# Optimization experiments

Hardware: AMD Instinct MI355X
Metric: run time of the kernel (lower is better)

Reference implementation:

```python
import jax, jax.numpy as jnp
from jax import lax
import numpy as np

VOCAB, EMB, HID, ENC, ATT, P = 10000, 512, 1024, 2048, 512, 196
B, T = 64, 160
PAD_IDX = 3

def setup_inputs() -> dict:
    key = jax.random.key(0)
    ks = jax.random.split(key, 20)
    s = 0.02
    emb = jax.random.normal(ks[0], (VOCAB, EMB), jnp.float32) * s
    emb = emb.at[PAD_IDX].set(0.0)
    return {
        'image_embedding': jax.random.normal(ks[1], (B, P, ENC), jnp.float32),
        'padded_sentence': jax.random.randint(ks[2], (B, T), 0, VOCAB),
        'enc_h': jax.random.normal(ks[3], (2, B, HID // 2), jnp.float32),
        'enc_c': jax.random.normal(ks[4], (2, B, HID // 2), jnp.float32),
        'sentence_lens': jax.random.randint(ks[5], (B,), 1, T + 1),
        'emb': emb,
        'Wea': jax.random.normal(ks[6], (ATT, ENC), jnp.float32) * s,
        'bea': jnp.zeros((ATT,), jnp.float32),
        'Wda': jax.random.normal(ks[7], (ATT, HID), jnp.float32) * s,
        'bda': jnp.zeros((ATT,), jnp.float32),
        'wfa': jax.random.normal(ks[8], (ATT,), jnp.float32) * s,
        'bfa': jnp.zeros((), jnp.float32),
        'Wfb': jax.random.normal(ks[9], (ENC, HID), jnp.float32) * s,
        'bfb': jnp.zeros((ENC,), jnp.float32),
        'Wih': jax.random.normal(ks[10], (4 * HID, EMB + ENC), jnp.float32) * s,
        'bih': jnp.zeros((4 * HID,), jnp.float32),
        'Whh': jax.random.normal(ks[11], (4 * HID, HID), jnp.float32) * s,
        'bhh': jnp.zeros((4 * HID,), jnp.float32),
    }


def reference(image_embedding, padded_sentence, enc_h, enc_c, sentence_lens,
              emb, Wea, bea, Wda, bda, wfa, bfa, Wfb, bfb, Wih, bih, Whh, bhh):
    Tn = padded_sentence.shape[1]
    # sort by descending length (replicates sentence_lens.sort(descending=True))
    idx = jnp.argsort(-sentence_lens)
    img = image_embedding[idx]                   # [B,P,E]
    sent = padded_sentence[idx]                  # [B,T]
    lens = sentence_lens[idx]                    # [B]
    h0 = jnp.concatenate([enc_h[-2], enc_h[-1]], axis=1)[idx]  # [B,HID]
    c0 = jnp.concatenate([enc_c[-2], enc_c[-1]], axis=1)[idx]
    emb_eff = emb.at[PAD_IDX].set(0.0)           # padding_idx=3
    x_emb = emb_eff[sent]                        # [B,T,EMB]
    # encoder projection is h-independent: hoist out of the scan
    att1 = jnp.einsum('bpe,ae->bpa', img, Wea) + bea  # [B,P,ATT]

    def step(carry, xt):
        h, c = carry
        x_t, t = xt
        active = (t < lens)[:, None]             # ragged mask
        att2 = h @ Wda.T + bda                   # [B,ATT]
        e = jax.nn.relu(att1 + att2[:, None, :]) @ wfa + bfa  # [B,P]
        alpha = jax.nn.softmax(e, axis=1)
        context = jnp.einsum('bp,bpe->be', alpha, img)        # [B,ENC]
        gate = jax.nn.sigmoid(h @ Wfb.T + bfb)
        inp = jnp.concatenate([x_t, gate * context], axis=1)  # [B,EMB+ENC]
        gates = inp @ Wih.T + bih + h @ Whh.T + bhh           # [B,4*HID]
        i, f, g, o = jnp.split(gates, 4, axis=1)
        c_new = jax.nn.sigmoid(f) * c + jax.nn.sigmoid(i) * jnp.tanh(g)
        h_new = jax.nn.sigmoid(o) * jnp.tanh(c_new)
        h = jnp.where(active, h_new, h)
        c = jnp.where(active, c_new, c)
        out_t = jnp.where(active, h_new, 0.0)
        alpha_t = jnp.where(active, alpha, 0.0)
        return (h, c), (out_t, alpha_t)

    (_, _), (outs, alphas) = lax.scan(
        step, (h0, c0), (jnp.swapaxes(x_emb, 0, 1), jnp.arange(Tn)))
    outputs = jnp.swapaxes(outs, 0, 1)           # [B,T,HID]
    alphas = jnp.swapaxes(alphas, 0, 1)          # [B,T,P]
    # replicate the original's final reindex (outputs[ordered_idx], not inverse)
    return outputs[idx], alphas[idx]
```

## Files before the change

kernel.cpp:

```cpp
#include <hip/hip_runtime.h>
#include <hip/hip_bf16.h>
#include <math.h>

#define B 64
#define T 160
#define P 196
#define ENC 2048
#define ATT 512
#define EMB 512
#define HID 1024
#define KTOT 3584
#define N2 2560
#define KT4 112
#define NTHR 1024
#define NBLK 256
#define NGRP 16
#define GRPSZ (NBLK/NGRP)

#define ARR_W 0
#define GD_W  16384
#define REL_W 17408

typedef __attribute__((ext_vector_type(8))) short bf16x8;
typedef __attribute__((ext_vector_type(4))) float f32x4;
typedef __attribute__((ext_vector_type(2))) float f32x2;

__device__ __forceinline__ float sigm(float x){ return 1.0f/(1.0f+__expf(-x)); }
__device__ __forceinline__ float bfu(short s){ return __uint_as_float(((unsigned)(unsigned short)s) << 16); }
__device__ __forceinline__ short f2bf(float x){ __hip_bfloat16 h = __float2bfloat16(x); return *(short*)&h; }

#if __has_builtin(__builtin_amdgcn_cvt_pk_f32_fp8)
#define FP8_DEC2(w, sel) __builtin_amdgcn_cvt_pk_f32_fp8((int)(w), (sel))
#else
__device__ __forceinline__ float fp8dec1(unsigned b){
    unsigned s = b >> 7, e = (b >> 3) & 15, m = b & 7;
    float v = e ? __uint_as_float(((e + 120u) << 23) | (m << 20)) : (float)(int)m * 0.001953125f;
    return s ? -v : v;
}
__device__ __forceinline__ f32x2 FP8_DEC2(unsigned w, int sel){
    unsigned h = sel ? (w >> 16) : (w & 0xFFFFu);
    f32x2 r; r.x = fp8dec1(h & 0xFF); r.y = fp8dec1(h >> 8);
    return r;
}
#endif

__device__ __forceinline__ unsigned char fp8enc(float x){
    unsigned bits = __float_as_uint(x);
    unsigned s = (bits >> 31) << 7;
    unsigned abits = bits & 0x7FFFFFFFu;
    float a = __uint_as_float(abits);
    if (a >= 448.f) return (unsigned char)(s | 0x7E);
    if (a < 0.0009765625f) return (unsigned char)s;
    int E = (int)(abits >> 23) - 127;
    if (E < -6){
        int q = (int)rintf(a * 512.0f);
        if (q >= 8) return (unsigned char)(s | 0x08);
        return (unsigned char)(s | q);
    }
    unsigned m23 = abits & 0x7FFFFFu;
    unsigned r = (m23 + 0x7FFFFu + ((m23 >> 20) & 1u)) >> 20;
    if (r >= 8){ r = 0; E++; }
    if (E > 8 || (E == 8 && r > 6)) return (unsigned char)(s | 0x7E);
    return (unsigned char)(s | ((unsigned)(E + 7) << 3) | r);
}

__device__ __forceinline__ float ldgf(const float* p){ return *(const volatile float*)p; }
__device__ __forceinline__ void stgf(float* p, float v){ *(volatile float*)p = v; }
__device__ __forceinline__ void stgu(unsigned* p, unsigned v){ *(volatile unsigned*)p = v; }
__device__ __forceinline__ unsigned pkbf(float a, float b){
    unsigned ua = (unsigned)__bfloat16_as_ushort(__float2bfloat16(a));
    unsigned ub = (unsigned)__bfloat16_as_ushort(__float2bfloat16(b));
    return ua | (ub << 16);
}

__device__ __forceinline__ void gbar_arrive(unsigned* bar, unsigned k){
    asm volatile("s_waitcnt vmcnt(0)" ::: "memory");
    __syncthreads();
    if (threadIdx.x == 0)
        *(volatile unsigned*)(bar + ARR_W + (unsigned)blockIdx.x*64) = k + 1u;
}
__device__ __forceinline__ void gbar_wait(unsigned* bar, unsigned k){
    int b = blockIdx.x, tid = threadIdx.x;
    if (b < NGRP){
        if (tid < 64){
            volatile unsigned* s = (volatile unsigned*)(bar + ARR_W + (unsigned)((tid & 15)*NGRP + b)*64);
            while (!__all(*s >= k + 1u)) __builtin_amdgcn_s_sleep(1);
            if (tid == 0) *(volatile unsigned*)(bar + GD_W + b*64) = k + 1u;
            volatile unsigned* g = (volatile unsigned*)(bar + GD_W + (tid & 15)*64);
            while (!__all(*g >= k + 1u)) __builtin_amdgcn_s_sleep(1);
            if (tid == 0) *(volatile unsigned*)(bar + REL_W + b*64) = k + 1u;
        }
    } else {
        if (tid == 0){
            volatile unsigned* r = (volatile unsigned*)(bar + REL_W + (b & (NGRP-1))*64);
            while (*r < k + 1u) __builtin_amdgcn_s_sleep(1);
        }
    }
    __syncthreads();
    asm volatile("" ::: "memory");
}
__device__ __forceinline__ void gbar(unsigned* bar, unsigned k){
    gbar_arrive(bar, k);
    gbar_wait(bar, k);
}

__global__ void k_sort(const int* lens, int* idx, int* rank, unsigned* barCnt, int* nAct){
    __shared__ int L[B];
    int i = threadIdx.x;
    L[i] = lens[i];
    for (int s = i; s < 288; s += B){
        int wofs = (s < 256) ? (ARR_W + s*64)
                 : (s < 272) ? (GD_W + (s-256)*64)
                             : (REL_W + (s-272)*64);
        barCnt[wofs] = 0u;
    }
    __syncthreads();
    int li = L[i];
    int r = 0;
    for (int j = 0; j < B; ++j){
        int lj = L[j];
        if (lj > li || (lj == li && j < i)) r++;
    }
    rank[i] = r;
    idx[r] = i;
    for (int tt = i; tt < T; tt += B){
        int c = 0;
        for (int j = 0; j < B; ++j) c += (L[j] > tt) ? 1 : 0;
        nAct[tt] = c;
    }
}

__global__ void k_init_hc(const float* enc_h, const float* enc_c, const int* idx,
                          float* h, float* c, __hip_bfloat16* hbR0){
    int j = blockIdx.x;
    int o = idx[j];
    for (int k = threadIdx.x; k < HID; k += blockDim.x){
        float hv = (k < 512) ? enc_h[o*512 + k] : enc_h[B*512 + o*512 + (k-512)];
        float cv = (k < 512) ? enc_c[o*512 + k] : enc_c[B*512 + o*512 + (k-512)];
        h[j*HID + k] = hv;
        c[j*HID + k] = cv;
        hbR0[j*HID + k] = __float2bfloat16(hv);
    }
}

__global__ void k_cvt_wcat(const float* Wih, const float* Whh, __hip_bfloat16* Wfrag){
    size_t i = (size_t)blockIdx.x*256 + threadIdx.x;
    int e = (int)(i & 7);
    size_t t2 = i >> 3;
    int lane = (int)(t2 & 63);
    size_t t3 = t2 >> 6;
    int kt = (int)(t3 % KT4);
    int strip = (int)(t3 / KT4);
    int n = strip*16 + (lane & 15);
    int r = (n & 3)*HID + (n >> 2);
    int k = kt*32 + (lane >> 4)*8 + e;
    float v = (k < EMB+ENC) ? Wih[(size_t)r*(EMB+ENC) + k]
                            : Whh[(size_t)r*HID + (k - EMB - ENC)];
    Wfrag[i] = __float2bfloat16(v);
}

__global__ void k_bsum(const float* bih, const float* bhh, float* bsum){
    int n = blockIdx.x*256 + threadIdx.x;
    int r = (n & 3)*HID + (n >> 2);
    bsum[n] = bih[r] + bhh[r];
}

__global__ void k_cvt_w2(const float* Wda, const float* bda, const float* Wfb, const float* bfb,
                         __hip_bfloat16* W2, float* bias2){
    int n = blockIdx.x;
    const float* src = (n < ATT) ? (Wda + (size_t)n*HID) : (Wfb + (size_t)(n-ATT)*HID);
    __hip_bfloat16* dst = W2 + (size_t)n*HID;
    for (int k = threadIdx.x; k < HID; k += 256) dst[k] = __float2bfloat16(src[k]);
    if (threadIdx.x == 0) bias2[n] = (n < ATT) ? bda[n] : bfb[n-ATT];
}

__global__ void k_cvt_emb(const float* emb, __hip_bfloat16* emb_bf){
    size_t i = (size_t)blockIdx.x*256 + threadIdx.x;
    emb_bf[i] = __float2bfloat16(emb[i]);
}

__global__ void k_cvt_wea(const float* Wea, __hip_bfloat16* Wea_bf){
    int n = blockIdx.x;
    for (int k = threadIdx.x; k < ENC; k += 256)
        Wea_bf[(size_t)n*ENC + k] = __float2bfloat16(Wea[(size_t)n*ENC + k]);
}

__global__ void k_cvt_img8(const float* img, const int* idx, unsigned char* img8){
    int j = blockIdx.y;
    int o = idx[j];
    size_t off = (size_t)blockIdx.x*256 + threadIdx.x;
    img8[(size_t)j*P*ENC + off] = fp8enc(img[(size_t)o*P*ENC + off]);
}

__global__ __launch_bounds__(256) void k_att1m(const float* img, const int* idx,
                                               const __hip_bfloat16* Wea_bf,
                                               const float* bea, __hip_bfloat16* att1w){
    int m0 = blockIdx.x * 64, n0 = blockIdx.y * 64;
    int tid = threadIdx.x, w = tid >> 6, l = tid & 63, lm = l & 15, lk = l >> 4;
    int g = m0 + 16*w + lm;
    int j = g / P, pp2 = g - j*P;
    int o = idx[j];
    const float* af = img + ((size_t)o*P + pp2)*ENC + 8*lk;
    const short* bp = (const short*)Wea_bf + (size_t)(n0 + lm)*ENC + 8*lk;
    f32x4 acc[4];
    #pragma unroll
    for (int nt=0; nt<4; ++nt) acc[nt] = (f32x4){0.f,0.f,0.f,0.f};
    #pragma unroll 4
    for (int kt = 0; kt < ENC/32; ++kt){
        float4 f0 = *(const float4*)(af + kt*32);
        float4 f1 = *(const float4*)(af + kt*32 + 4);
        bf16x8 a;
        a[0]=f2bf(f0.x); a[1]=f2bf(f0.y); a[2]=f2bf(f0.z); a[3]=f2bf(f0.w);
        a[4]=f2bf(f1.x); a[5]=f2bf(f1.y); a[6]=f2bf(f1.z); a[7]=f2bf(f1.w);
        #pragma unroll
        for (int nt=0; nt<4; ++nt){
            bf16x8 bb = *(const bf16x8*)(bp + (size_t)nt*16*ENC + kt*32);
            acc[nt] = __builtin_amdgcn_mfma_f32_16x16x32_bf16(a, bb, acc[nt], 0,0,0);
        }
    }
    #pragma unroll
    for (int nt=0; nt<4; ++nt){
        int n = n0 + nt*16 + lm;
        float bv = bea[n];
        #pragma unroll
        for (int r=0; r<4; ++r){
            int m = m0 + 16*w + 4*lk + r;
            att1w[(size_t)m*ATT + n] = __float2bfloat16(acc[nt][r] + bv);
        }
    }
}

struct SP {
    const __hip_bfloat16 *att1w, *emb_bf, *Wfrag, *W2;
    const unsigned char *img8;
    const float *bsum, *bias2, *wfa, *bfa;
    const int *sent, *idx, *rank, *lens, *nAct;
    float *D2;
    __hip_bfloat16 *gcR, *hbR;
    float *hF0, *hF1, *cW;
    float *outH, *outA;
    unsigned *barCnt;
};

__global__ __launch_bounds__(1024, 4) void k_scan(SP p){
    __shared__ short WcatL[KT4*64*8];
    __shared__ union {
        struct { float Dp[4][64][17]; float hS[64][4]; int tokL[64], lensL[64], wLs[64]; } gem;
        struct { float att2L[512]; float wfaL[512]; float red[1024]; float aL[208]; float ctxP[8][512]; } p23;
    } sh;

    int b = blockIdx.x, tid = threadIdx.x;
    int w = tid >> 6, l = tid & 63, lm = l & 15, lk = l >> 4;
    unsigned bk = 0;

    {
        const bf16x8* src = (const bf16x8*)((const short*)p.Wfrag + (size_t)b*KT4*64*8);
        bf16x8* dst = (bf16x8*)WcatL;
        #pragma unroll
        for (int i = 0; i < KT4*64/NTHR; ++i) dst[tid + i*NTHR] = src[tid + i*NTHR];
    }
    __syncthreads();

    float bfa0 = p.bfa[0];

    for (int t = 0; t < T; ++t){
        const __hip_bfloat16* hbIn = p.hbR + (size_t)t*B*HID;
        __hip_bfloat16*       hbOut = p.hbR + (size_t)(t+1)*B*HID;
        const __hip_bfloat16* gcT  = p.gcR + (size_t)t*B*ENC;
        const float* hFIn = (t & 1) ? p.hF1 : p.hF0;
        float*       hFOut = (t & 1) ? p.hF0 : p.hF1;
        int nAct = p.nAct[t];

        if (b < N2/16){
            int n0 = b*16;
            int rt = w & 3, kq = w >> 2;
            if (16*rt < nAct){
                const short* ap = (const short*)hbIn + (size_t)(16*rt + lm)*HID + kq*256 + 8*lk;
                const short* bp = (const short*)p.W2 + (size_t)(n0 + lm)*HID + kq*256 + 8*lk;
                f32x4 acc = {0.f,0.f,0.f,0.f};
                #pragma unroll
                for (int kt = 0; kt < 8; ++kt){
                    bf16x8 a = *(const bf16x8*)(ap + kt*32);
                    bf16x8 bb = *(const bf16x8*)(bp + kt*32);
                    acc = __builtin_amdgcn_mfma_f32_16x16x32_bf16(a, bb, acc, 0,0,0);
                }
                #pragma unroll
                for (int r=0; r<4; ++r) sh.gem.Dp[kq][16*rt + 4*lk + r][lm] = acc[r];
            }
            __syncthreads();
            int m = tid >> 4, nl = tid & 15;
            if (m < nAct){
                stgf(&p.D2[m*N2 + n0 + nl],
                     sh.gem.Dp[0][m][nl] + sh.gem.Dp[1][m][nl]
                   + sh.gem.Dp[2][m][nl] + sh.gem.Dp[3][m][nl] + p.bias2[n0 + nl]);
            }
        }
        gbar(p.barCnt, bk); bk++;

        int jj = b & 63, qq = b >> 6;
        int oo = p.idx[jj], wjj = p.rank[jj], ljj = p.lens[oo];
        {
            if (t < ljj){
                if (tid < 512){
                    sh.p23.att2L[tid] = ldgf(&p.D2[jj*N2 + tid]);
                    sh.p23.wfaL[tid]  = p.wfa[tid];
                }
                __syncthreads();

                int pp = tid & 255, ah = tid >> 8;
                float acc = 0.f;
                if (pp < P){
                    const short* ar = (const short*)p.att1w + (size_t)(jj*P + pp)*ATT + ah*128;
                    #pragma unroll 8
                    for (int k8 = 0; k8 < 16; ++k8){
                        bf16x8 v = *(const bf16x8*)(ar + k8*8);
                        #pragma unroll
                        for (int z=0; z<8; ++z){
                            int a = ah*128 + k8*8 + z;
                            acc += fmaxf(bfu(v[z]) + sh.p23.att2L[a], 0.f) * sh.p23.wfaL[a];
                        }
                    }
                }
                sh.p23.red[tid] = acc;
                __syncthreads();
                float e = -1e30f;
                if (tid < P) e = sh.p23.red[tid] + sh.p23.red[tid+256] + sh.p23.red[tid+512] + sh.p23.red[tid+768] + bfa0;
                __syncthreads();
                sh.p23.red[tid] = (tid < P) ? e : -1e30f;
                __syncthreads();
                for (int s = 512; s > 0; s >>= 1){
                    if (tid < s) sh.p23.red[tid] = fmaxf(sh.p23.red[tid], sh.p23.red[tid+s]);
                    __syncthreads();
                }
                float m = sh.p23.red[0];
                __syncthreads();
                float ex = (tid < P) ? __expf(e - m) : 0.f;
                sh.p23.red[tid] = ex;
                __syncthreads();
                for (int s = 512; s > 0; s >>= 1){
                    if (tid < s) sh.p23.red[tid] += sh.p23.red[tid+s];
                    __syncthreads();
                }
                float ssum = sh.p23.red[0];
                if (tid < P) sh.p23.aL[tid] = ex / ssum;
                if (tid >= P && tid < 208) sh.p23.aL[tid] = 0.f;
                __syncthreads();

                const unsigned char* ib = p.img8 + (size_t)jj*P*ENC + qq*512 + l*8;
                float a8[8];
                #pragma unroll
                for (int z=0; z<8; ++z) a8[z] = 0.f;
                #pragma unroll 4
                for (int i = 0; i < 13; ++i){
                    int pp2 = w + 16*i;
                    int pr = (pp2 < P) ? pp2 : 0;
                    uint2 v = *(const uint2*)(ib + (size_t)pr*ENC);
                    float al = sh.p23.aL[pp2];
                    f32x2 f01 = FP8_DEC2(v.x, 0);
                    f32x2 f23 = FP8_DEC2(v.x, 1);
                    f32x2 f45 = FP8_DEC2(v.y, 0);
                    f32x2 f67 = FP8_DEC2(v.y, 1);
                    a8[0] += al * f01.x; a8[1] += al * f01.y;
                    a8[2] += al * f23.x; a8[3] += al * f23.y;
                    a8[4] += al * f45.x; a8[5] += al * f45.y;
                    a8[6] += al * f67.x; a8[7] += al * f67.y;
                }
                if (w < 8){
                    #pragma unroll
                    for (int z=0; z<8; ++z) sh.p23.ctxP[w][l*8+z] = a8[z];
                }
                __syncthreads();
                if (w >= 8){
                    #pragma unroll
                    for (int z=0; z<8; ++z) sh.p23.ctxP[w-8][l*8+z] += a8[z];
                }
                __syncthreads();
                if (tid < 256){
                    int d0 = 2*tid;
                    float c0 = 0.f, c1 = 0.f;
                    #pragma unroll
                    for (int r=0; r<8; ++r){ c0 += sh.p23.ctxP[r][d0]; c1 += sh.p23.ctxP[r][d0+1]; }
                    int eg0 = qq*512 + d0;
                    float g0 = sigm(ldgf(&p.D2[jj*N2 + ATT + eg0]));
                    float g1 = sigm(ldgf(&p.D2[jj*N2 + ATT + eg0 + 1]));
                    stgu((unsigned*)((short*)gcT + jj*ENC + eg0), pkbf(g0*c0, g1*c1));
                }
            }
        }
        gbar_arrive(p.barCnt, bk);

        if (qq == 0 && tid < P){
            float av = (t < ljj) ? sh.p23.aL[tid] : 0.f;
            p.outA[((size_t)(wjj*T + t))*P + tid] = av;
        }
        __syncthreads();

        if (tid < 64){
            int o = p.idx[tid];
            sh.gem.tokL[tid] = p.sent[o*T + t];
            sh.gem.lensL[tid] = p.lens[o];
            sh.gem.wLs[tid] = p.rank[tid];
        }
        __syncthreads();
        {
            int rt = w & 3, kq = w >> 2;
            bool act = (16*rt < nAct);
            int mrow = 16*rt + lm;
            f32x4 acc = {0.f,0.f,0.f,0.f};
            const short* aEmb = 0; const short* aGc = 0; const short* aH = 0;
            const bf16x8* BL = (const bf16x8*)WcatL;
            if (act){
                int tok = sh.gem.tokL[mrow];
                aEmb = (const short*)p.emb_bf + (size_t)tok*EMB + 8*lk;
                aGc  = (const short*)gcT + (size_t)mrow*ENC + 8*lk;
                aH   = (const short*)hbIn + (size_t)mrow*HID + 8*lk;
                if (kq == 0){
                    #pragma unroll 8
                    for (int kt = 0; kt < 16; ++kt){
                        bf16x8 a = *(const bf16x8*)(aEmb + kt*32);
                        acc = __builtin_amdgcn_mfma_f32_16x16x32_bf16(a, BL[kt*64 + l], acc, 0,0,0);
                    }
                } else if (kq == 2){
                    #pragma unroll
                    for (int kt = 80; kt < 84; ++kt){
                        bf16x8 a = *(const bf16x8*)(aH + (kt-80)*32);
                        acc = __builtin_amdgcn_mfma_f32_16x16x32_bf16(a, BL[kt*64 + l], acc, 0,0,0);
                    }
                } else if (kq == 3){
                    #pragma unroll 7
                    for (int kt = 84; kt < 112; ++kt){
                        bf16x8 a = *(const bf16x8*)(aH + (kt-80)*32);
                        acc = __builtin_amdgcn_mfma_f32_16x16x32_bf16(a, BL[kt*64 + l], acc, 0,0,0);
                    }
                }
            }
            gbar_wait(p.barCnt, bk); bk++;

            if (act){
                if (kq == 0){
                    #pragma unroll 6
                    for (int kt = 16; kt < 28; ++kt){
                        bf16x8 a = *(const bf16x8*)(aGc + (kt-16)*32);
                        acc = __builtin_amdgcn_mfma_f32_16x16x32_bf16(a, BL[kt*64 + l], acc, 0,0,0);
                    }
                } else if (kq == 1){
                    #pragma unroll 7
                    for (int kt = 28; kt < 56; ++kt){
                        bf16x8 a = *(const bf16x8*)(aGc + (kt-16)*32);
                        acc = __builtin_amdgcn_mfma_f32_16x16x32_bf16(a, BL[kt*64 + l], acc, 0,0,0);
                    }
                } else if (kq == 2){
                    #pragma unroll 6
                    for (int kt = 56; kt < 80; ++kt){
                        bf16x8 a = *(const bf16x8*)(aGc + (kt-16)*32);
                        acc = __builtin_amdgcn_mfma_f32_16x16x32_bf16(a, BL[kt*64 + l], acc, 0,0,0);
                    }
                }
                #pragma unroll
                for (int r=0; r<4; ++r) sh.gem.Dp[kq][16*rt + 4*lk + r][lm] = acc[r];
            }
        }
        __syncthreads();

        int j2 = tid & 63, du = tid >> 6;
        int u = 4*b + du;
        float cNew = 0.f, hNew = 0.f, hKeep = 0.f, cOld = 0.f;
        bool active = false;
        if (tid < 256){
            float g4[4];
            #pragma unroll
            for (int g=0; g<4; ++g){
                int nl = 4*du + g;
                g4[g] = sh.gem.Dp[0][j2][nl] + sh.gem.Dp[1][j2][nl]
                      + sh.gem.Dp[2][j2][nl] + sh.gem.Dp[3][j2][nl] + p.bsum[16*b + nl];
            }
            float ig = sigm(g4[0]), fg = sigm(g4[1]), gg = tanhf(g4[2]), og = sigm(g4[3]);
            cOld = p.cW[j2*HID + u];
            cNew = fg*cOld + ig*gg;
            hNew = og*tanhf(cNew);
            active = (t < sh.gem.lensL[j2]);
            float hOld = hFIn[j2*HID + u];
            hKeep = active ? hNew : hOld;
            sh.gem.hS[j2][du] = hKeep;
        }
        __syncthreads();
        if (tid < 128){
            int jb = tid & 63, dp = tid >> 6;
            int u0 = 4*b + 2*dp;
            stgu((unsigned*)((short*)hbOut + jb*HID + u0),
                 pkbf(sh.gem.hS[jb][2*dp], sh.gem.hS[jb][2*dp+1]));
        }
        gbar_arrive(p.barCnt, bk);
        if (tid < 256){
            p.cW[j2*HID + u] = active ? cNew : cOld;
            hFOut[j2*HID + u] = hKeep;
            p.outH[((size_t)sh.gem.wLs[j2]*T + t)*HID + u] = active ? hNew : 0.f;
        }
        gbar_wait(p.barCnt, bk); bk++;
    }
}

extern "C" void kernel_launch(void* const* d_in, const int* in_sizes, int n_in,
                              void* d_out, int out_size, void* d_ws, size_t ws_size,
                              hipStream_t stream) {
    const float* img   = (const float*)d_in[0];
    const int*   sent  = (const int*)  d_in[1];
    const float* enc_h = (const float*)d_in[2];
    const float* enc_c = (const float*)d_in[3];
    const int*   lens  = (const int*)  d_in[4];
    const float* emb   = (const float*)d_in[5];
    const float* Wea   = (const float*)d_in[6];
    const float* bea   = (const float*)d_in[7];
    const float* Wda   = (const float*)d_in[8];
    const float* bda   = (const float*)d_in[9];
    const float* wfa   = (const float*)d_in[10];
    const float* bfa   = (const float*)d_in[11];
    const float* Wfb   = (const float*)d_in[12];
    const float* bfb   = (const float*)d_in[13];
    const float* Wih   = (const float*)d_in[14];
    const float* bih   = (const float*)d_in[15];
    const float* Whh   = (const float*)d_in[16];
    const float* bhh   = (const float*)d_in[17];

    float* outH = (float*)d_out;
    float* outA = outH + (size_t)B*T*HID;

    char* wsb = (char*)d_ws;
    size_t off = 0;
    int* idxW  = (int*)(wsb + off); off += 256;
    int* rankW = (int*)(wsb + off); off += 256;
    int* nActW = (int*)(wsb + off); off += 1024;
    unsigned* barCnt = (unsigned*)(wsb + off); off += 131072;
    __hip_bfloat16* att1w = (__hip_bfloat16*)(wsb + off); off += (size_t)B*P*ATT*2;
    unsigned char* img8 = (unsigned char*)(wsb + off); off += (size_t)B*P*ENC;
    __hip_bfloat16* emb_bf= (__hip_bfloat16*)(wsb + off); off += (size_t)10000*EMB*2;
    __hip_bfloat16* Wfrag = (__hip_bfloat16*)(wsb + off); off += (size_t)4*HID*KTOT*2;
    __hip_bfloat16* W2    = (__hip_bfloat16*)(wsb + off); off += (size_t)N2*HID*2;
    __hip_bfloat16* Wea_bf= (__hip_bfloat16*)(wsb + off); off += (size_t)ATT*ENC*2;
    float* bsum  = (float*)(wsb + off); off += 4*HID*4;
    float* bias2 = (float*)(wsb + off); off += N2*4;
    float* hA    = (float*)(wsb + off); off += B*HID*4;
    float* hB    = (float*)(wsb + off); off += B*HID*4;
    float* cWs   = (float*)(wsb + off); off += B*HID*4;
    float* D2    = (float*)(wsb + off); off += (size_t)B*N2*4;
    __hip_bfloat16* gcR = (__hip_bfloat16*)(wsb + off); off += (size_t)T*B*ENC*2;
    __hip_bfloat16* hbR = (__hip_bfloat16*)(wsb + off); off += (size_t)(T+1)*B*HID*2;

    k_sort<<<1, 64, 0, stream>>>(lens, idxW, rankW, barCnt, nActW);
    k_init_hc<<<B, 256, 0, stream>>>(enc_h, enc_c, idxW, hA, cWs, hbR);
    k_cvt_wcat<<<57344, 256, 0, stream>>>(Wih, Whh, Wfrag);
    k_bsum<<<16, 256, 0, stream>>>(bih, bhh, bsum);
    k_cvt_w2<<<N2, 256, 0, stream>>>(Wda, bda, Wfb, bfb, W2, bias2);
    k_cvt_emb<<<20000, 256, 0, stream>>>(emb, emb_bf);
    k_cvt_wea<<<ATT, 256, 0, stream>>>(Wea, Wea_bf);
    k_cvt_img8<<<dim3(P*ENC/256, B), 256, 0, stream>>>(img, idxW, img8);
    k_att1m<<<dim3((B*P)/64, ATT/64), 256, 0, stream>>>(img, idxW, Wea_bf, bea, att1w);

    SP sp;
    sp.att1w = att1w; sp.img8 = img8; sp.emb_bf = emb_bf; sp.Wfrag = Wfrag; sp.W2 = W2;
    sp.bsum = bsum; sp.bias2 = bias2; sp.wfa = wfa; sp.bfa = bfa;
    sp.sent = sent; sp.idx = idxW; sp.rank = rankW; sp.lens = lens; sp.nAct = nActW;
    sp.D2 = D2; sp.gcR = gcR; sp.hbR = hbR;
    sp.hF0 = hA; sp.hF1 = hB; sp.cW = cWs;
    sp.outH = outH; sp.outA = outA;
    sp.barCnt = barCnt;

    void* args[] = { &sp };
    hipLaunchCooperativeKernel(reinterpret_cast<void*>(k_scan), dim3(NBLK), dim3(NTHR),
                               args, 0, stream);
}
```

Before: 6.884 ms.

## Replace grid-wide barriers with per-producer dataflow flags and wave-shuffle softmax

The three hierarchical grid barriers per timestep are replaced by per-block monotonic progress flags. Each consumer wave polls only the blocks that produce the data it needs: the h slices for the recurrent GEMM, the D2 columns for attention, and all gated-context producers before the LSTM gate GEMM. Blocks can therefore start a phase as soon as their own inputs are ready instead of waiting for every block at every phase. The softmax max and sum tree reductions over 1024 shared-memory slots are also replaced with 64-lane shuffles plus a 4-entry combine, removing many __syncthreads. Correctness now relies on the flag ordering to cover the write-after-read hazards on D2 and hbR.

```diff
diff --git a/kernel.cpp b/kernel.cpp
--- a/kernel.cpp
+++ b/kernel.cpp
@@ -14,12 +14,6 @@
 #define KT4 112
 #define NTHR 1024
 #define NBLK 256
-#define NGRP 16
-#define GRPSZ (NBLK/NGRP)
-
-#define ARR_W 0
-#define GD_W  16384
-#define REL_W 17408
 
 typedef __attribute__((ext_vector_type(8))) short bf16x8;
 typedef __attribute__((ext_vector_type(4))) float f32x4;
@@ -73,47 +67,37 @@
     return ua | (ub << 16);
 }
 
-__device__ __forceinline__ void gbar_arrive(unsigned* bar, unsigned k){
+__device__ __forceinline__ void arrive(unsigned* bar, unsigned pi){
     asm volatile("s_waitcnt vmcnt(0)" ::: "memory");
     __syncthreads();
     if (threadIdx.x == 0)
-        *(volatile unsigned*)(bar + ARR_W + (unsigned)blockIdx.x*64) = k + 1u;
-}
-__device__ __forceinline__ void gbar_wait(unsigned* bar, unsigned k){
-    int b = blockIdx.x, tid = threadIdx.x;
-    if (b < NGRP){
-        if (tid < 64){
-            volatile unsigned* s = (volatile unsigned*)(bar + ARR_W + (unsigned)((tid & 15)*NGRP + b)*64);
-            while (!__all(*s >= k + 1u)) __builtin_amdgcn_s_sleep(1);
-            if (tid == 0) *(volatile unsigned*)(bar + GD_W + b*64) = k + 1u;
-            volatile unsigned* g = (volatile unsigned*)(bar + GD_W + (tid & 15)*64);
-            while (!__all(*g >= k + 1u)) __builtin_amdgcn_s_sleep(1);
-            if (tid == 0) *(volatile unsigned*)(bar + REL_W + b*64) = k + 1u;
-        }
-    } else {
-        if (tid == 0){
-            volatile unsigned* r = (volatile unsigned*)(bar + REL_W + (b & (NGRP-1))*64);
-            while (*r < k + 1u) __builtin_amdgcn_s_sleep(1);
-        }
-    }
-    __syncthreads();
+        *(volatile unsigned*)(bar + (unsigned)blockIdx.x*16) = pi;
+}
+__device__ __forceinline__ void wave_wait(unsigned* bar, int flagIdx, unsigned target){
+    volatile unsigned* s = (volatile unsigned*)(bar + flagIdx*16);
+    while (!__all(*s >= target)) __builtin_amdgcn_s_sleep(1);
     asm volatile("" ::: "memory");
 }
-__device__ __forceinline__ void gbar(unsigned* bar, unsigned k){
-    gbar_arrive(bar, k);
-    gbar_wait(bar, k);
+__device__ __forceinline__ void wave_wait_all(unsigned* bar, unsigned target){
+    int l = threadIdx.x & 63;
+    volatile unsigned* s0 = (volatile unsigned*)(bar + l*16);
+    volatile unsigned* s1 = (volatile unsigned*)(bar + (l+64)*16);
+    volatile unsigned* s2 = (volatile unsigned*)(bar + (l+128)*16);
+    volatile unsigned* s3 = (volatile unsigned*)(bar + (l+192)*16);
+    for (;;){
+        unsigned a = *s0, b = *s1, c = *s2, d = *s3;
+        unsigned mn = min(min(a,b), min(c,d));
+        if (__all(mn >= target)) break;
+        __builtin_amdgcn_s_sleep(1);
+    }
+    asm volatile("" ::: "memory");
 }
 
 __global__ void k_sort(const int* lens, int* idx, int* rank, unsigned* barCnt, int* nAct){
     __shared__ int L[B];
     int i = threadIdx.x;
     L[i] = lens[i];
-    for (int s = i; s < 288; s += B){
-        int wofs = (s < 256) ? (ARR_W + s*64)
-                 : (s < 272) ? (GD_W + (s-256)*64)
-                             : (REL_W + (s-272)*64);
-        barCnt[wofs] = 0u;
-    }
+    for (int s = i; s < 256; s += B) barCnt[s*16] = 0u;
     __syncthreads();
     int li = L[i];
     int r = 0;
@@ -251,7 +235,6 @@
 
     int b = blockIdx.x, tid = threadIdx.x;
     int w = tid >> 6, l = tid & 63, lm = l & 15, lk = l >> 4;
-    unsigned bk = 0;
 
     {
         const bf16x8* src = (const bf16x8*)((const short*)p.Wfrag + (size_t)b*KT4*64*8);
@@ -262,6 +245,7 @@
     __syncthreads();
 
     float bfa0 = p.bfa[0];
+    int jj = b & 63, qq = b >> 6;
 
     for (int t = 0; t < T; ++t){
         const __hip_bfloat16* hbIn = p.hbR + (size_t)t*B*HID;
@@ -270,10 +254,12 @@
         const float* hFIn = (t & 1) ? p.hF1 : p.hF0;
         float*       hFOut = (t & 1) ? p.hF0 : p.hF1;
         int nAct = p.nAct[t];
+        unsigned pi0 = 3u*(unsigned)t;
 
         if (b < N2/16){
             int n0 = b*16;
             int rt = w & 3, kq = w >> 2;
+            wave_wait(p.barCnt, 64*kq + l, pi0);
             if (16*rt < nAct){
                 const short* ap = (const short*)hbIn + (size_t)(16*rt + lm)*HID + kq*256 + 8*lk;
                 const short* bp = (const short*)p.W2 + (size_t)(n0 + lm)*HID + kq*256 + 8*lk;
@@ -294,100 +280,106 @@
                      sh.gem.Dp[0][m][nl] + sh.gem.Dp[1][m][nl]
                    + sh.gem.Dp[2][m][nl] + sh.gem.Dp[3][m][nl] + p.bias2[n0 + nl]);
             }
-        }
-        gbar(p.barCnt, bk); bk++;
-
-        int jj = b & 63, qq = b >> 6;
-        int oo = p.idx[jj], wjj = p.rank[jj], ljj = p.lens[oo];
-        {
-            if (t < ljj){
-                if (tid < 512){
-                    sh.p23.att2L[tid] = ldgf(&p.D2[jj*N2 + tid]);
-                    sh.p23.wfaL[tid]  = p.wfa[tid];
+            arrive(p.barCnt, pi0 + 1u);
+        }
+
+        if (w == 0){
+            int fi = (l < 32) ? l : (32*qq + l);
+            wave_wait(p.barCnt, fi, pi0 + 1u);
+        }
+        __syncthreads();
+
+        int ljj = p.lens[p.idx[jj]];
+        int wjj = p.rank[jj];
+        if (t < ljj){
+            if (tid < 512){
+                sh.p23.att2L[tid] = ldgf(&p.D2[jj*N2 + tid]);
+                sh.p23.wfaL[tid]  = p.wfa[tid];
+            }
+            __syncthreads();
+
+            int pp = tid & 255, ah = tid >> 8;
+            float acc = 0.f;
+            if (pp < P){
+                const short* ar = (const short*)p.att1w + (size_t)(jj*P + pp)*ATT + ah*128;
+                #pragma unroll 8
+                for (int k8 = 0; k8 < 16; ++k8){
+                    bf16x8 v = *(const bf16x8*)(ar + k8*8);
+                    #pragma unroll
+                    for (int z=0; z<8; ++z){
+                        int a = ah*128 + k8*8 + z;
+                        acc += fmaxf(bfu(v[z]) + sh.p23.att2L[a], 0.f) * sh.p23.wfaL[a];
+                    }
                 }
-                __syncthreads();
-
-                int pp = tid & 255, ah = tid >> 8;
-                float acc = 0.f;
-                if (pp < P){
-                    const short* ar = (const short*)p.att1w + (size_t)(jj*P + pp)*ATT + ah*128;
-                    #pragma unroll 8
-                    for (int k8 = 0; k8 < 16; ++k8){
-                        bf16x8 v = *(const bf16x8*)(ar + k8*8);
-                        #pragma unroll
-                        for (int z=0; z<8; ++z){
-                            int a = ah*128 + k8*8 + z;
-                            acc += fmaxf(bfu(v[z]) + sh.p23.att2L[a], 0.f) * sh.p23.wfaL[a];
-                        }
-                    }
-                }
-                sh.p23.red[tid] = acc;
-                __syncthreads();
-                float e = -1e30f;
-                if (tid < P) e = sh.p23.red[tid] + sh.p23.red[tid+256] + sh.p23.red[tid+512] + sh.p23.red[tid+768] + bfa0;
-                __syncthreads();
-                sh.p23.red[tid] = (tid < P) ? e : -1e30f;
-                __syncthreads();
-                for (int s = 512; s > 0; s >>= 1){
-                    if (tid < s) sh.p23.red[tid] = fmaxf(sh.p23.red[tid], sh.p23.red[tid+s]);
-                    __syncthreads();
-                }
-                float m = sh.p23.red[0];
-                __syncthreads();
-                float ex = (tid < P) ? __expf(e - m) : 0.f;
-                sh.p23.red[tid] = ex;
-                __syncthreads();
-                for (int s = 512; s > 0; s >>= 1){
-                    if (tid < s) sh.p23.red[tid] += sh.p23.red[tid+s];
-                    __syncthreads();
-                }
-                float ssum = sh.p23.red[0];
-                if (tid < P) sh.p23.aL[tid] = ex / ssum;
-                if (tid >= P && tid < 208) sh.p23.aL[tid] = 0.f;
-                __syncthreads();
-
-                const unsigned char* ib = p.img8 + (size_t)jj*P*ENC + qq*512 + l*8;
-                float a8[8];
-                #pragma unroll
-                for (int z=0; z<8; ++z) a8[z] = 0.f;
-                #pragma unroll 4
-                for (int i = 0; i < 13; ++i){
-                    int pp2 = w + 16*i;
-                    int pr = (pp2 < P) ? pp2 : 0;
-                    uint2 v = *(const uint2*)(ib + (size_t)pr*ENC);
-                    float al = sh.p23.aL[pp2];
-                    f32x2 f01 = FP8_DEC2(v.x, 0);
-                    f32x2 f23 = FP8_DEC2(v.x, 1);
-                    f32x2 f45 = FP8_DEC2(v.y, 0);
-                    f32x2 f67 = FP8_DEC2(v.y, 1);
-                    a8[0] += al * f01.x; a8[1] += al * f01.y;
-                    a8[2] += al * f23.x; a8[3] += al * f23.y;
-                    a8[4] += al * f45.x; a8[5] += al * f45.y;
-                    a8[6] += al * f67.x; a8[7] += al * f67.y;
-                }
-                if (w < 8){
-                    #pragma unroll
-                    for (int z=0; z<8; ++z) sh.p23.ctxP[w][l*8+z] = a8[z];
-                }
-                __syncthreads();
-                if (w >= 8){
-                    #pragma unroll
-                    for (int z=0; z<8; ++z) sh.p23.ctxP[w-8][l*8+z] += a8[z];
-                }
-                __syncthreads();
-                if (tid < 256){
-                    int d0 = 2*tid;
-                    float c0 = 0.f, c1 = 0.f;
-                    #pragma unroll
-                    for (int r=0; r<8; ++r){ c0 += sh.p23.ctxP[r][d0]; c1 += sh.p23.ctxP[r][d0+1]; }
-                    int eg0 = qq*512 + d0;
-                    float g0 = sigm(ldgf(&p.D2[jj*N2 + ATT + eg0]));
-                    float g1 = sigm(ldgf(&p.D2[jj*N2 + ATT + eg0 + 1]));
-                    stgu((unsigned*)((short*)gcT + jj*ENC + eg0), pkbf(g0*c0, g1*c1));
-                }
-            }
-        }
-        gbar_arrive(p.barCnt, bk);
+            }
+            sh.p23.red[tid] = acc;
+            __syncthreads();
+            float e = -1e30f;
+            if (tid < P) e = sh.p23.red[tid] + sh.p23.red[tid+256] + sh.p23.red[tid+512] + sh.p23.red[tid+768] + bfa0;
+            float* sm  = &sh.p23.red[976];
+            float* sm2 = &sh.p23.red[984];
+            if (tid < 256){
+                float mv = e;
+                #pragma unroll
+                for (int off = 32; off; off >>= 1) mv = fmaxf(mv, __shfl_xor(mv, off, 64));
+                if (l == 0) sm[w] = mv;
+            }
+            __syncthreads();
+            float m = fmaxf(fmaxf(sm[0], sm[1]), fmaxf(sm[2], sm[3]));
+            float ex = (tid < P) ? __expf(e - m) : 0.f;
+            if (tid < 256){
+                float sv = ex;
+                #pragma unroll
+                for (int off = 32; off; off >>= 1) sv += __shfl_xor(sv, off, 64);
+                if (l == 0) sm2[w] = sv;
+            }
+            __syncthreads();
+            float ssum = sm2[0] + sm2[1] + sm2[2] + sm2[3];
+            if (tid < P) sh.p23.aL[tid] = ex / ssum;
+            if (tid >= P && tid < 208) sh.p23.aL[tid] = 0.f;
+            __syncthreads();
+
+            const unsigned char* ib = p.img8 + (size_t)jj*P*ENC + qq*512 + l*8;
+            float a8[8];
+            #pragma unroll
+            for (int z=0; z<8; ++z) a8[z] = 0.f;
+            #pragma unroll 4
+            for (int i = 0; i < 13; ++i){
+                int pp2 = w + 16*i;
+                int pr = (pp2 < P) ? pp2 : 0;
+                uint2 v = *(const uint2*)(ib + (size_t)pr*ENC);
+                float al = sh.p23.aL[pp2];
+                f32x2 f01 = FP8_DEC2(v.x, 0);
+                f32x2 f23 = FP8_DEC2(v.x, 1);
+                f32x2 f45 = FP8_DEC2(v.y, 0);
+                f32x2 f67 = FP8_DEC2(v.y, 1);
+                a8[0] += al * f01.x; a8[1] += al * f01.y;
+                a8[2] += al * f23.x; a8[3] += al * f23.y;
+                a8[4] += al * f45.x; a8[5] += al * f45.y;
+                a8[6] += al * f67.x; a8[7] += al * f67.y;
+            }
+            if (w < 8){
+                #pragma unroll
+                for (int z=0; z<8; ++z) sh.p23.ctxP[w][l*8+z] = a8[z];
+            }
+            __syncthreads();
+            if (w >= 8){
+                #pragma unroll
+                for (int z=0; z<8; ++z) sh.p23.ctxP[w-8][l*8+z] += a8[z];
+            }
+            __syncthreads();
+            if (tid < 256){
+                int d0 = 2*tid;
+                float c0 = 0.f, c1 = 0.f;
+                #pragma unroll
+                for (int r=0; r<8; ++r){ c0 += sh.p23.ctxP[r][d0]; c1 += sh.p23.ctxP[r][d0+1]; }
+                int eg0 = qq*512 + d0;
+                float g0 = sigm(ldgf(&p.D2[jj*N2 + ATT + eg0]));
+                float g1 = sigm(ldgf(&p.D2[jj*N2 + ATT + eg0 + 1]));
+                stgu((unsigned*)((short*)gcT + jj*ENC + eg0), pkbf(g0*c0, g1*c1));
+            }
+        }
+        arrive(p.barCnt, pi0 + 2u);
 
         if (qq == 0 && tid < P){
             float av = (t < ljj) ? sh.p23.aL[tid] : 0.f;
@@ -434,7 +426,8 @@
                     }
                 }
             }
-            gbar_wait(p.barCnt, bk); bk++;
+            if (tid < 64) wave_wait_all(p.barCnt, pi0 + 2u);
+            __syncthreads();
 
             if (act){
                 if (kq == 0){
@@ -490,13 +483,12 @@
             stgu((unsigned*)((short*)hbOut + jb*HID + u0),
                  pkbf(sh.gem.hS[jb][2*dp], sh.gem.hS[jb][2*dp+1]));
         }
-        gbar_arrive(p.barCnt, bk);
+        arrive(p.barCnt, pi0 + 3u);
         if (tid < 256){
             p.cW[j2*HID + u] = active ? cNew : cOld;
             hFOut[j2*HID + u] = hKeep;
             p.outH[((size_t)sh.gem.wLs[j2]*T + t)*HID + u] = active ? hNew : 0.f;
         }
-        gbar_wait(p.barCnt, bk); bk++;
     }
 }
 
@@ -530,7 +522,7 @@
     int* idxW  = (int*)(wsb + off); off += 256;
     int* rankW = (int*)(wsb + off); off += 256;
     int* nActW = (int*)(wsb + off); off += 1024;
-    unsigned* barCnt = (unsigned*)(wsb + off); off += 131072;
+    unsigned* barCnt = (unsigned*)(wsb + off); off += 32768;
     __hip_bfloat16* att1w = (__hip_bfloat16*)(wsb + off); off += (size_t)B*P*ATT*2;
     unsigned char* img8 = (unsigned char*)(wsb + off); off += (size_t)B*P*ENC;
     __hip_bfloat16* emb_bf= (__hip_bfloat16*)(wsb + off); off += (size_t)10000*EMB*2;
```

After: 6.733 ms. -2.2%, faster.
